# Optimization experiments

Measured on AMD Instinct MI355X. Metric: run time of the kernel, lower is better.

## Reference

```python
import itertools
import jax, jax.numpy as jnp
import numpy as np

ACTION_BLADES = (0, 5, 6, 7, 8, 9, 10, 15)  # even subalgebra of Cl(3,0,1)
INPUT_BLADES = (11, 12, 13)                  # trivector point coords e012,e013,e023
E123_IDX = 14                                # homogeneous coordinate blade


def _build_cayley():
    """Cayley table M[i,j,k]: e_i * e_j = sum_k M[i,j,k] e_k for metric [0,1,1,1]."""
    metric = [0, 1, 1, 1]
    blades = [()]
    for g in range(1, 5):
        blades += list(itertools.combinations(range(4), g))
    idx = {b: i for i, b in enumerate(blades)}
    M = np.zeros((16, 16, 16), np.float32)
    for i, a in enumerate(blades):
        for j, b in enumerate(blades):
            arr = list(a) + list(b)
            sign = 1
            n = len(arr)
            for p in range(n):            # bubble sort, counting swaps
                for q in range(n - 1):
                    if arr[q] > arr[q + 1]:
                        arr[q], arr[q + 1] = arr[q + 1], arr[q]
                        sign = -sign
            res, k = [], 0
            while k < len(arr):           # contract repeated generators with metric
                if k + 1 < len(arr) and arr[k] == arr[k + 1]:
                    sign *= metric[arr[k]]
                    k += 2
                else:
                    res.append(arr[k])
                    k += 1
            if sign != 0:
                M[i, j, idx[tuple(res)]] += sign
    grades = np.array([len(b) for b in blades])
    rev = ((-1.0) ** (grades * (grades - 1) // 2)).astype(np.float32)  # reverse signs
    return M, rev


CAYLEY_NP, REVERSE_NP = _build_cayley()


def setup_inputs() -> dict:
    key = jax.random.key(0)
    k1, k2, k3, k4 = jax.random.split(key, 4)
    B, I, O = 4096, 512, 512
    x = jax.random.normal(k1, (B, I, 3), jnp.float32)
    weight = jax.random.normal(k2, (O, I), jnp.float32) * (1.0 / np.sqrt(I))
    action = jax.random.normal(k3, (O, I, 8), jnp.float32) * 0.1
    embed_e0 = jax.random.normal(k4, (I, 1), jnp.float32)
    return {"x": x, "weight": weight, "action": action, "embed_e0": embed_e0}


def reference(x, weight, action, embed_e0):
    M = jnp.asarray(CAYLEY_NP)
    rev = jnp.asarray(REVERSE_NP)
    o, i, _ = action.shape
    b = x.shape[0]
    ab = jnp.array(ACTION_BLADES)
    ib = jnp.array(INPUT_BLADES)
    # embed action into full 16-blade multivector; k_ = reverse(k)
    k = jnp.zeros((o, i, 16), x.dtype).at[..., ab].set(action)
    k_ = k * rev
    # embed input points as trivectors, set e123 component from embed_e0
    xf = jnp.zeros((b, i, 16), x.dtype).at[..., ib].set(x)
    xf = xf.at[..., E123_IDX].set(jnp.broadcast_to(embed_e0[:, 0], (b, i)))
    # left/right geometric-product kernels (unflattened)
    k_l = jnp.einsum('ijk,pqi->jpkq', M, k)    # (16, o, 16, i)
    k_r = jnp.einsum('ijk,pqk->jpiq', M, k_)   # (16, o, 16, i)
    # sandwich conjugation + channel mixing, fused einsum
    out = jnp.einsum('oi,poqi,qori,bir->bop', weight, k_r, k_l, xf)
    return out[..., ib]


if __name__ == "__main__":
    out = reference(**setup_inputs())
    print(out.shape)
```

## Files before the change

### kernel.cpp

```cpp
#include <hip/hip_runtime.h>
#include <hip/hip_bf16.h>


#define B_DIM 4096
#define I_DIM 512
#define O_DIM 512
#define N_DIM (O_DIM * 3)
#define K_DIM (I_DIM * 3)
#define NT (K_DIM / 64)

typedef __attribute__((ext_vector_type(8))) short bf16x8;
typedef __attribute__((ext_vector_type(4))) float f32x4;

__device__ __forceinline__ unsigned short f2bf(float f) {
    unsigned u = __float_as_uint(f);
    unsigned r = (u + 0x7fffu + ((u >> 16) & 1u)) >> 16;
    return (unsigned short)r;
}

__device__ __forceinline__ void gload_lds16(const void* g, void* l) {
    __builtin_amdgcn_global_load_lds(
        (const __attribute__((address_space(1))) unsigned*)g,
        (__attribute__((address_space(3))) unsigned*)l, 16, 0, 0);
}

struct Cayley {
    float M[16][16][16];
    float rev[16];
    constexpr Cayley() : M{}, rev{} {
        const unsigned masks[16] = {0u, 1u, 2u, 4u, 8u, 3u, 5u, 9u, 6u, 10u,
                                    12u, 7u, 11u, 13u, 14u, 15u};
        int idx_of[16] = {};
        for (int i = 0; i < 16; ++i) idx_of[masks[i]] = i;
        const int metric[4] = {0, 1, 1, 1};
        for (int i = 0; i < 16; ++i) {
            unsigned a = masks[i];
            for (int j = 0; j < 16; ++j) {
                unsigned b = masks[j];
                int swaps = 0;
                for (int jb = 0; jb < 4; ++jb)
                    if ((b >> jb) & 1u)
                        for (int ia = jb + 1; ia < 4; ++ia)
                            if ((a >> ia) & 1u) ++swaps;
                int sign = (swaps & 1) ? -1 : 1;
                unsigned common = a & b;
                for (int g = 0; g < 4; ++g)
                    if ((common >> g) & 1u) sign *= metric[g];
                if (sign != 0) M[i][j][idx_of[a ^ b]] += (float)sign;
            }
            int grade = 0;
            for (int g = 0; g < 4; ++g) grade += (int)((a >> g) & 1u);
            rev[i] = ((grade * (grade - 1) / 2) % 2) ? -1.f : 1.f;
        }
    }
};
constexpr Cayley CAY{};

__global__ __launch_bounds__(256) void build_w(const float* __restrict__ weight,
                                               const float* __restrict__ action,
                                               unsigned short* __restrict__ Bw) {
    const int t = blockIdx.x * 256 + threadIdx.x;
    const int o = t >> 9;
    const int i = t & 511;

    float a[8];
    const float* ap = action + (size_t)t * 8;
#pragma unroll
    for (int j = 0; j < 8; ++j) a[j] = ap[j];

    float kv[16], kr[16];
#pragma unroll
    for (int j = 0; j < 16; ++j) { kv[j] = 0.f; kr[j] = 0.f; }
    constexpr int AB[8] = {0, 5, 6, 7, 8, 9, 10, 15};
#pragma unroll
    for (int j = 0; j < 8; ++j) {
        kv[AB[j]] = a[j];
        kr[AB[j]] = a[j] * CAY.rev[AB[j]];
    }

    constexpr int PB[3] = {11, 12, 13};
    constexpr int RB[3] = {11, 12, 13};

    float Am[3][16];
#pragma unroll
    for (int pp = 0; pp < 3; ++pp)
#pragma unroll
        for (int q = 0; q < 16; ++q) {
            float s = 0.f;
#pragma unroll
            for (int tt = 0; tt < 16; ++tt) s += CAY.M[q][PB[pp]][tt] * kr[tt];
            Am[pp][q] = s;
        }

    float Bm[16][3];
#pragma unroll
    for (int q = 0; q < 16; ++q)
#pragma unroll
        for (int rr = 0; rr < 3; ++rr) {
            float s = 0.f;
#pragma unroll
            for (int m = 0; m < 16; ++m) s += CAY.M[m][q][RB[rr]] * kv[m];
            Bm[q][rr] = s;
        }

    const float w = weight[t];
#pragma unroll
    for (int pp = 0; pp < 3; ++pp) {
        float r0 = 0.f, r1 = 0.f, r2 = 0.f;
#pragma unroll
        for (int q = 0; q < 16; ++q) {
            r0 += Am[pp][q] * Bm[q][0];
            r1 += Am[pp][q] * Bm[q][1];
            r2 += Am[pp][q] * Bm[q][2];
        }
        unsigned short* bp = Bw + (size_t)(o * 3 + pp) * K_DIM + i * 3;
        bp[0] = f2bf(w * r0);
        bp[1] = f2bf(w * r1);
        bp[2] = f2bf(w * r2);
    }
}

__global__ __launch_bounds__(64) void build_bias(const float* __restrict__ weight,
                                                 const float* __restrict__ action,
                                                 const float* __restrict__ e0,
                                                 float* __restrict__ bias) {
    const int o = blockIdx.x;
    const int lane = threadIdx.x;
    constexpr int AB[8] = {0, 5, 6, 7, 8, 9, 10, 15};
    constexpr int PB[3] = {11, 12, 13};

    float s0 = 0.f, s1 = 0.f, s2 = 0.f;
#pragma unroll
    for (int ii = 0; ii < 8; ++ii) {
        const int i = lane + ii * 64;
        const int t = o * I_DIM + i;
        float a[8];
        const float* ap = action + (size_t)t * 8;
#pragma unroll
        for (int j = 0; j < 8; ++j) a[j] = ap[j];
        float kv[16], kr[16];
#pragma unroll
        for (int j = 0; j < 16; ++j) { kv[j] = 0.f; kr[j] = 0.f; }
#pragma unroll
        for (int j = 0; j < 8; ++j) {
            kv[AB[j]] = a[j];
            kr[AB[j]] = a[j] * CAY.rev[AB[j]];
        }
        float Bm3[16];
#pragma unroll
        for (int q = 0; q < 16; ++q) {
            float s = 0.f;
#pragma unroll
            for (int m = 0; m < 16; ++m) s += CAY.M[m][q][14] * kv[m];
            Bm3[q] = s;
        }
        float T3[3];
#pragma unroll
        for (int pp = 0; pp < 3; ++pp) {
            float acc = 0.f;
#pragma unroll
            for (int q = 0; q < 16; ++q) {
                float am = 0.f;
#pragma unroll
                for (int tt = 0; tt < 16; ++tt) am += CAY.M[q][PB[pp]][tt] * kr[tt];
                acc += am * Bm3[q];
            }
            T3[pp] = acc;
        }
        const float we = weight[t] * e0[i];
        s0 += we * T3[0];
        s1 += we * T3[1];
        s2 += we * T3[2];
    }
#pragma unroll
    for (int off = 32; off; off >>= 1) {
        s0 += __shfl_down(s0, off, 64);
        s1 += __shfl_down(s1, off, 64);
        s2 += __shfl_down(s2, off, 64);
    }
    if (lane == 0) {
        bias[o * 3 + 0] = s0;
        bias[o * 3 + 1] = s1;
        bias[o * 3 + 2] = s2;
    }
}

__global__ __launch_bounds__(256) void pack_x(const float* __restrict__ x,
                                              unsigned short* __restrict__ A) {
    const size_t t = (size_t)blockIdx.x * 256 + threadIdx.x;
    const float4* xp = (const float4*)(x + t * 8);
    const float4 v0 = xp[0], v1 = xp[1];
    const float xs[8] = {v0.x, v0.y, v0.z, v0.w, v1.x, v1.y, v1.z, v1.w};
    unsigned short ov[8];
#pragma unroll
    for (int q = 0; q < 8; ++q) ov[q] = f2bf(xs[q]);
    *(uint4*)(A + t * 8) = *(const uint4*)ov;
}

__global__ __launch_bounds__(256) void gemm_bf16(const unsigned short* __restrict__ A,
                                                 const unsigned short* __restrict__ Bw,
                                                 const float* __restrict__ bias,
                                                 float* __restrict__ C) {
    __shared__ unsigned short As0[64 * 64], As1[64 * 64];
    __shared__ unsigned short Bs0[128 * 64], Bs1[128 * 64];

    const int tid = threadIdx.x;
    const int wave = tid >> 6, lane = tid & 63;

    const int bid = blockIdx.x;
    const int swz = (bid & 7) * 96 + (bid >> 3);
    const int mt = swz / 12, nt = swz - mt * 12;
    const int m0 = mt * 64, n0 = nt * 128;
    const int wr = wave >> 1, wc = wave & 1;

    const int sA0 = tid, sA1 = tid + 256;
    const unsigned short* aSrc0 =
        A + (size_t)(m0 + (sA0 >> 3)) * K_DIM + (((sA0 & 7) ^ ((sA0 >> 3) & 7)) * 8);
    const unsigned short* aSrc1 =
        A + (size_t)(m0 + (sA1 >> 3)) * K_DIM + (((sA1 & 7) ^ ((sA1 >> 3) & 7)) * 8);
    const int aOff0 = (0 * 256 + wave * 64) * 8;
    const int aOff1 = (1 * 256 + wave * 64) * 8;

    const unsigned short* bSrc[4];
    int bOff[4];
#pragma unroll
    for (int q = 0; q < 4; ++q) {
        const int s = tid + q * 256;
        bSrc[q] = Bw + (size_t)(n0 + (s >> 3)) * K_DIM +
                  (((s & 7) ^ ((s >> 3) & 7)) * 8);
        bOff[q] = (q * 256 + wave * 64) * 8;
    }

    const int frow = lane & 15;
    const int g0 = lane >> 4;

    f32x4 acc[2][4] = {};

#define STAGE(AS, BS, K0)                                   \
    do {                                                    \
        gload_lds16(aSrc0 + (K0), (AS) + aOff0);            \
        gload_lds16(aSrc1 + (K0), (AS) + aOff1);            \
        _Pragma("unroll")                                   \
        for (int q = 0; q < 4; ++q)                         \
            gload_lds16(bSrc[q] + (K0), (BS) + bOff[q]);    \
    } while (0)

#define COMPUTE(AS, BS)                                                        \
    do {                                                                       \
        bf16x8 af[2][2], bfr[2][4];                                            \
        _Pragma("unroll")                                                      \
        for (int kh = 0; kh < 2; ++kh) {                                       \
            _Pragma("unroll")                                                  \
            for (int mi = 0; mi < 2; ++mi) {                                   \
                const int r = wr * 32 + mi * 16 + frow;                        \
                af[kh][mi] =                                                   \
                    *(const bf16x8*)&(AS)[r * 64 + ((g0 + kh * 4) ^ (r & 7)) * 8]; \
            }                                                                  \
            _Pragma("unroll")                                                  \
            for (int ni = 0; ni < 4; ++ni) {                                   \
                const int r = wc * 64 + ni * 16 + frow;                        \
                bfr[kh][ni] =                                                  \
                    *(const bf16x8*)&(BS)[r * 64 + ((g0 + kh * 4) ^ (r & 7)) * 8]; \
            }                                                                  \
        }                                                                      \
        _Pragma("unroll")                                                      \
        for (int kh = 0; kh < 2; ++kh)                                         \
            _Pragma("unroll")                                                  \
            for (int mi = 0; mi < 2; ++mi)                                     \
                _Pragma("unroll")                                              \
                for (int ni = 0; ni < 4; ++ni)                                 \
                    acc[mi][ni] = __builtin_amdgcn_mfma_f32_16x16x32_bf16(     \
                        af[kh][mi], bfr[kh][ni], acc[mi][ni], 0, 0, 0);        \
    } while (0)

    STAGE(As0, Bs0, 0);
    __syncthreads();

    for (int t = 0; t < NT - 2; t += 2) {
        STAGE(As1, Bs1, (t + 1) * 64);
        COMPUTE(As0, Bs0);
        __syncthreads();
        STAGE(As0, Bs0, (t + 2) * 64);
        COMPUTE(As1, Bs1);
        __syncthreads();
    }
    STAGE(As1, Bs1, (NT - 1) * 64);
    COMPUTE(As0, Bs0);
    __syncthreads();
    COMPUTE(As1, Bs1);

#undef STAGE
#undef COMPUTE

    const int crow = (lane >> 4) * 4;
    const int ccol = lane & 15;
#pragma unroll
    for (int mi = 0; mi < 2; ++mi)
#pragma unroll
        for (int ni = 0; ni < 4; ++ni) {
            const int n = n0 + wc * 64 + ni * 16 + ccol;
            const float bv = bias[n];
            float* cp = C + (size_t)(m0 + wr * 32 + mi * 16 + crow) * N_DIM + n;
#pragma unroll
            for (int j = 0; j < 4; ++j) cp[(size_t)j * N_DIM] = acc[mi][ni][j] + bv;
        }
}

extern "C" void kernel_launch(void* const* d_in, const int* in_sizes, int n_in,
                              void* d_out, int out_size, void* d_ws, size_t ws_size,
                              hipStream_t stream) {
    const float* x      = (const float*)d_in[0];
    const float* weight = (const float*)d_in[1];
    const float* action = (const float*)d_in[2];
    const float* e0     = (const float*)d_in[3];
    float* out = (float*)d_out;

    unsigned short* Bw = (unsigned short*)d_ws;
    unsigned short* Ap = Bw + (size_t)N_DIM * K_DIM;
    float* bias = (float*)(Ap + (size_t)B_DIM * K_DIM);

    hipLaunchKernelGGL(build_w, dim3((O_DIM * I_DIM) / 256), dim3(256), 0, stream,
                       weight, action, Bw);
    hipLaunchKernelGGL(build_bias, dim3(O_DIM), dim3(64), 0, stream,
                       weight, action, e0, bias);
    hipLaunchKernelGGL(pack_x, dim3((B_DIM * K_DIM / 8) / 256), dim3(256), 0, stream,
                       x, Ap);
    hipLaunchKernelGGL(gemm_bf16, dim3(768), dim3(256), 0, stream,
                       Ap, Bw, bias, out);
}
```

Baseline: 51.00 us.

## Fuse weight and bias builders; use eight waves per GEMM block

The separate build_w and build_bias kernels are merged into one kernel with one block per output channel. It computes the sandwich coefficients once, extends the right factor to four columns so the e123 bias term comes out alongside the weights, and reduces the bias across waves through shared memory. This removes one launch and the duplicated action reads and Cayley math. The GEMM keeps its 64x128 tile but runs 512 threads, so each wave owns a 32x32 sub-tile instead of 32x64; this raises wave count and cuts per-wave registers, at the cost of more LDS fragment reads per MFMA.

```diff
diff --git a/kernel.cpp b/kernel.cpp
--- a/kernel.cpp
+++ b/kernel.cpp
@@ -58,86 +58,30 @@
 
 __global__ __launch_bounds__(256) void build_w(const float* __restrict__ weight,
                                                const float* __restrict__ action,
-                                               unsigned short* __restrict__ Bw) {
-    const int t = blockIdx.x * 256 + threadIdx.x;
-    const int o = t >> 9;
-    const int i = t & 511;
-
-    float a[8];
-    const float* ap = action + (size_t)t * 8;
-#pragma unroll
-    for (int j = 0; j < 8; ++j) a[j] = ap[j];
-
-    float kv[16], kr[16];
-#pragma unroll
-    for (int j = 0; j < 16; ++j) { kv[j] = 0.f; kr[j] = 0.f; }
-    constexpr int AB[8] = {0, 5, 6, 7, 8, 9, 10, 15};
-#pragma unroll
-    for (int j = 0; j < 8; ++j) {
-        kv[AB[j]] = a[j];
-        kr[AB[j]] = a[j] * CAY.rev[AB[j]];
-    }
-
-    constexpr int PB[3] = {11, 12, 13};
-    constexpr int RB[3] = {11, 12, 13};
-
-    float Am[3][16];
-#pragma unroll
-    for (int pp = 0; pp < 3; ++pp)
-#pragma unroll
-        for (int q = 0; q < 16; ++q) {
-            float s = 0.f;
-#pragma unroll
-            for (int tt = 0; tt < 16; ++tt) s += CAY.M[q][PB[pp]][tt] * kr[tt];
-            Am[pp][q] = s;
-        }
-
-    float Bm[16][3];
-#pragma unroll
-    for (int q = 0; q < 16; ++q)
-#pragma unroll
-        for (int rr = 0; rr < 3; ++rr) {
-            float s = 0.f;
-#pragma unroll
-            for (int m = 0; m < 16; ++m) s += CAY.M[m][q][RB[rr]] * kv[m];
-            Bm[q][rr] = s;
-        }
-
-    const float w = weight[t];
-#pragma unroll
-    for (int pp = 0; pp < 3; ++pp) {
-        float r0 = 0.f, r1 = 0.f, r2 = 0.f;
-#pragma unroll
-        for (int q = 0; q < 16; ++q) {
-            r0 += Am[pp][q] * Bm[q][0];
-            r1 += Am[pp][q] * Bm[q][1];
-            r2 += Am[pp][q] * Bm[q][2];
-        }
-        unsigned short* bp = Bw + (size_t)(o * 3 + pp) * K_DIM + i * 3;
-        bp[0] = f2bf(w * r0);
-        bp[1] = f2bf(w * r1);
-        bp[2] = f2bf(w * r2);
-    }
-}
-
-__global__ __launch_bounds__(64) void build_bias(const float* __restrict__ weight,
-                                                 const float* __restrict__ action,
-                                                 const float* __restrict__ e0,
-                                                 float* __restrict__ bias) {
+                                               const float* __restrict__ e0,
+                                               unsigned short* __restrict__ Bw,
+                                               float* __restrict__ bias) {
     const int o = blockIdx.x;
-    const int lane = threadIdx.x;
+    const int tid = threadIdx.x;
+    const int wave = tid >> 6, lane = tid & 63;
+    __shared__ float red[4][3];
+
     constexpr int AB[8] = {0, 5, 6, 7, 8, 9, 10, 15};
     constexpr int PB[3] = {11, 12, 13};
-
-    float s0 = 0.f, s1 = 0.f, s2 = 0.f;
-#pragma unroll
-    for (int ii = 0; ii < 8; ++ii) {
-        const int i = lane + ii * 64;
+    constexpr int RB[4] = {11, 12, 13, 14};
+
+    float sb[3] = {0.f, 0.f, 0.f};
+
+#pragma unroll
+    for (int s = 0; s < 2; ++s) {
+        const int i = tid * 2 + s;
         const int t = o * I_DIM + i;
+
         float a[8];
         const float* ap = action + (size_t)t * 8;
 #pragma unroll
         for (int j = 0; j < 8; ++j) a[j] = ap[j];
+
         float kv[16], kr[16];
 #pragma unroll
         for (int j = 0; j < 16; ++j) { kv[j] = 0.f; kr[j] = 0.f; }
@@ -146,42 +90,63 @@
             kv[AB[j]] = a[j];
             kr[AB[j]] = a[j] * CAY.rev[AB[j]];
         }
-        float Bm3[16];
-#pragma unroll
-        for (int q = 0; q < 16; ++q) {
-            float s = 0.f;
-#pragma unroll
-            for (int m = 0; m < 16; ++m) s += CAY.M[m][q][14] * kv[m];
-            Bm3[q] = s;
-        }
-        float T3[3];
+
+        float Am[3][16];
+#pragma unroll
+        for (int pp = 0; pp < 3; ++pp)
+#pragma unroll
+            for (int q = 0; q < 16; ++q) {
+                float sum = 0.f;
+#pragma unroll
+                for (int tt = 0; tt < 16; ++tt) sum += CAY.M[q][PB[pp]][tt] * kr[tt];
+                Am[pp][q] = sum;
+            }
+
+        float Bm[16][4];
+#pragma unroll
+        for (int q = 0; q < 16; ++q)
+#pragma unroll
+            for (int rr = 0; rr < 4; ++rr) {
+                float sum = 0.f;
+#pragma unroll
+                for (int m = 0; m < 16; ++m) sum += CAY.M[m][q][RB[rr]] * kv[m];
+                Bm[q][rr] = sum;
+            }
+
+        const float w = weight[t];
+        const float e0i = e0[i];
 #pragma unroll
         for (int pp = 0; pp < 3; ++pp) {
-            float acc = 0.f;
+            float r0 = 0.f, r1 = 0.f, r2 = 0.f, r3 = 0.f;
 #pragma unroll
             for (int q = 0; q < 16; ++q) {
-                float am = 0.f;
-#pragma unroll
-                for (int tt = 0; tt < 16; ++tt) am += CAY.M[q][PB[pp]][tt] * kr[tt];
-                acc += am * Bm3[q];
-            }
-            T3[pp] = acc;
-        }
-        const float we = weight[t] * e0[i];
-        s0 += we * T3[0];
-        s1 += we * T3[1];
-        s2 += we * T3[2];
-    }
+                r0 += Am[pp][q] * Bm[q][0];
+                r1 += Am[pp][q] * Bm[q][1];
+                r2 += Am[pp][q] * Bm[q][2];
+                r3 += Am[pp][q] * Bm[q][3];
+            }
+            unsigned short* bp = Bw + (size_t)(o * 3 + pp) * K_DIM + i * 3;
+            bp[0] = f2bf(w * r0);
+            bp[1] = f2bf(w * r1);
+            bp[2] = f2bf(w * r2);
+            sb[pp] += w * r3 * e0i;
+        }
+    }
+
 #pragma unroll
     for (int off = 32; off; off >>= 1) {
-        s0 += __shfl_down(s0, off, 64);
-        s1 += __shfl_down(s1, off, 64);
-        s2 += __shfl_down(s2, off, 64);
+#pragma unroll
+        for (int pp = 0; pp < 3; ++pp) sb[pp] += __shfl_down(sb[pp], off, 64);
     }
     if (lane == 0) {
-        bias[o * 3 + 0] = s0;
-        bias[o * 3 + 1] = s1;
-        bias[o * 3 + 2] = s2;
+#pragma unroll
+        for (int pp = 0; pp < 3; ++pp) red[wave][pp] = sb[pp];
+    }
+    __syncthreads();
+    if (tid == 0) {
+#pragma unroll
+        for (int pp = 0; pp < 3; ++pp)
+            bias[o * 3 + pp] = red[0][pp] + red[1][pp] + red[2][pp] + red[3][pp];
     }
 }
 
@@ -197,10 +162,11 @@
     *(uint4*)(A + t * 8) = *(const uint4*)ov;
 }
 
-__global__ __launch_bounds__(256) void gemm_bf16(const unsigned short* __restrict__ A,
-                                                 const unsigned short* __restrict__ Bw,
-                                                 const float* __restrict__ bias,
-                                                 float* __restrict__ C) {
+__global__ __launch_bounds__(512, 6) void gemm_bf16(
+        const unsigned short* __restrict__ A,
+        const unsigned short* __restrict__ Bw,
+        const float* __restrict__ bias,
+        float* __restrict__ C) {
     __shared__ unsigned short As0[64 * 64], As1[64 * 64];
     __shared__ unsigned short Bs0[128 * 64], Bs1[128 * 64];
 
@@ -211,43 +177,38 @@
     const int swz = (bid & 7) * 96 + (bid >> 3);
     const int mt = swz / 12, nt = swz - mt * 12;
     const int m0 = mt * 64, n0 = nt * 128;
-    const int wr = wave >> 1, wc = wave & 1;
-
-    const int sA0 = tid, sA1 = tid + 256;
-    const unsigned short* aSrc0 =
-        A + (size_t)(m0 + (sA0 >> 3)) * K_DIM + (((sA0 & 7) ^ ((sA0 >> 3) & 7)) * 8);
-    const unsigned short* aSrc1 =
-        A + (size_t)(m0 + (sA1 >> 3)) * K_DIM + (((sA1 & 7) ^ ((sA1 >> 3) & 7)) * 8);
-    const int aOff0 = (0 * 256 + wave * 64) * 8;
-    const int aOff1 = (1 * 256 + wave * 64) * 8;
-
-    const unsigned short* bSrc[4];
-    int bOff[4];
-#pragma unroll
-    for (int q = 0; q < 4; ++q) {
-        const int s = tid + q * 256;
+    const int wr = wave >> 2, wc = wave & 3;
+
+    const int sA = tid;
+    const unsigned short* aSrc =
+        A + (size_t)(m0 + (sA >> 3)) * K_DIM + (((sA & 7) ^ ((sA >> 3) & 7)) * 8);
+    const int aOff = tid * 16 / 2;
+
+    const unsigned short* bSrc[2];
+    int bOff[2];
+#pragma unroll
+    for (int q = 0; q < 2; ++q) {
+        const int s = tid + q * 512;
         bSrc[q] = Bw + (size_t)(n0 + (s >> 3)) * K_DIM +
                   (((s & 7) ^ ((s >> 3) & 7)) * 8);
-        bOff[q] = (q * 256 + wave * 64) * 8;
+        bOff[q] = s * 8;
     }
 
     const int frow = lane & 15;
     const int g0 = lane >> 4;
 
-    f32x4 acc[2][4] = {};
+    f32x4 acc[2][2] = {};
 
 #define STAGE(AS, BS, K0)                                   \
     do {                                                    \
-        gload_lds16(aSrc0 + (K0), (AS) + aOff0);            \
-        gload_lds16(aSrc1 + (K0), (AS) + aOff1);            \
-        _Pragma("unroll")                                   \
-        for (int q = 0; q < 4; ++q)                         \
-            gload_lds16(bSrc[q] + (K0), (BS) + bOff[q]);    \
+        gload_lds16(aSrc + (K0), (AS) + aOff);              \
+        gload_lds16(bSrc[0] + (K0), (BS) + bOff[0]);        \
+        gload_lds16(bSrc[1] + (K0), (BS) + bOff[1]);        \
     } while (0)
 
 #define COMPUTE(AS, BS)                                                        \
     do {                                                                       \
-        bf16x8 af[2][2], bfr[2][4];                                            \
+        bf16x8 af[2][2], bfr[2][2];                                            \
         _Pragma("unroll")                                                      \
         for (int kh = 0; kh < 2; ++kh) {                                       \
             _Pragma("unroll")                                                  \
@@ -257,8 +218,8 @@
                     *(const bf16x8*)&(AS)[r * 64 + ((g0 + kh * 4) ^ (r & 7)) * 8]; \
             }                                                                  \
             _Pragma("unroll")                                                  \
-            for (int ni = 0; ni < 4; ++ni) {                                   \
-                const int r = wc * 64 + ni * 16 + frow;                        \
+            for (int ni = 0; ni < 2; ++ni) {                                   \
+                const int r = wc * 32 + ni * 16 + frow;                        \
                 bfr[kh][ni] =                                                  \
                     *(const bf16x8*)&(BS)[r * 64 + ((g0 + kh * 4) ^ (r & 7)) * 8]; \
             }                                                                  \
@@ -268,7 +229,7 @@
             _Pragma("unroll")                                                  \
             for (int mi = 0; mi < 2; ++mi)                                     \
                 _Pragma("unroll")                                              \
-                for (int ni = 0; ni < 4; ++ni)                                 \
+                for (int ni = 0; ni < 2; ++ni)                                 \
                     acc[mi][ni] = __builtin_amdgcn_mfma_f32_16x16x32_bf16(     \
                         af[kh][mi], bfr[kh][ni], acc[mi][ni], 0, 0, 0);        \
     } while (0)
@@ -297,8 +258,8 @@
 #pragma unroll
     for (int mi = 0; mi < 2; ++mi)
 #pragma unroll
-        for (int ni = 0; ni < 4; ++ni) {
-            const int n = n0 + wc * 64 + ni * 16 + ccol;
+        for (int ni = 0; ni < 2; ++ni) {
+            const int n = n0 + wc * 32 + ni * 16 + ccol;
             const float bv = bias[n];
             float* cp = C + (size_t)(m0 + wr * 32 + mi * 16 + crow) * N_DIM + n;
 #pragma unroll
@@ -319,12 +280,10 @@
     unsigned short* Ap = Bw + (size_t)N_DIM * K_DIM;
     float* bias = (float*)(Ap + (size_t)B_DIM * K_DIM);
 
-    hipLaunchKernelGGL(build_w, dim3((O_DIM * I_DIM) / 256), dim3(256), 0, stream,
-                       weight, action, Bw);
-    hipLaunchKernelGGL(build_bias, dim3(O_DIM), dim3(64), 0, stream,
-                       weight, action, e0, bias);
+    hipLaunchKernelGGL(build_w, dim3(O_DIM), dim3(256), 0, stream,
+                       weight, action, e0, Bw, bias);
     hipLaunchKernelGGL(pack_x, dim3((B_DIM * K_DIM / 8) / 256), dim3(256), 0, stream,
                        x, Ap);
-    hipLaunchKernelGGL(gemm_bf16, dim3(768), dim3(256), 0, stream,
+    hipLaunchKernelGGL(gemm_bf16, dim3(768), dim3(512), 0, stream,
                        Ap, Bw, bias, out);
 }
```

New measurement: 44.66 us. 1.14x faster.
